# Kernel optimization log

Measured on AMD Instinct MI355X. Metric: run time of the kernel, lower is better.

The kernel has to match this reference:

```python
import jax, jax.numpy as jnp
import numpy as np

N = 50000      # nodes
E = 800000     # edges
F_IN = 128     # numInputFeatures
HID = 64       # numHiddenLayerFeatures
C = 40         # numClasses


def setup_inputs() -> dict:
    key = jax.random.key(0)
    ks = jax.random.split(key, 24)
    def nrm(k, shape, s=0.05):
        return jax.random.normal(k, shape, jnp.float32) * s
    return {
        "x": jax.random.normal(ks[0], (N, F_IN), jnp.float32),
        "edge_index": jax.random.randint(ks[1], (2, E), 0, N, jnp.int64),
        "w": jax.random.normal(ks[2], (3,), jnp.float32),  # ensemble weights
        # GCNConv
        "W_gcn": nrm(ks[3], (F_IN, HID)), "b_gcn": jnp.zeros((HID,), jnp.float32),
        # SAGEConv (lin_l on aggregated neighbors w/ bias, lin_r on root no bias)
        "Wl_sage": nrm(ks[4], (F_IN, HID)), "bl_sage": jnp.zeros((HID,), jnp.float32),
        "Wr_sage": nrm(ks[5], (F_IN, HID)),
        # GATConv heads=1
        "W_gat": nrm(ks[6], (F_IN, HID)), "att_src": nrm(ks[7], (HID,)),
        "att_dst": nrm(ks[8], (HID,)), "b_gat": jnp.zeros((HID,), jnp.float32),
        # TransformerConv heads=1 (hidden -> classes)
        "Wq": nrm(ks[9], (HID, C)), "bq": jnp.zeros((C,), jnp.float32),
        "Wk": nrm(ks[10], (HID, C)), "bk": jnp.zeros((C,), jnp.float32),
        "Wv": nrm(ks[11], (HID, C)), "bv": jnp.zeros((C,), jnp.float32),
        "Wskip": nrm(ks[12], (HID, C)), "bskip": jnp.zeros((C,), jnp.float32),
    }


def _segment_softmax(e, seg, num_segments):
    m = jax.ops.segment_max(e, seg, num_segments=num_segments)
    ex = jnp.exp(e - m[seg])
    s = jax.ops.segment_sum(ex, seg, num_segments=num_segments)
    return ex / (s[seg] + 1e-16)


def _gcn(x, src, dst, W, b):
    h = x @ W                                        # [N, HID]
    loop = jnp.arange(N, dtype=src.dtype)
    s = jnp.concatenate([src, loop]); d = jnp.concatenate([dst, loop])
    deg = jax.ops.segment_sum(jnp.ones_like(d, jnp.float32), d, num_segments=N)
    dinv = jnp.where(deg > 0, jax.lax.rsqrt(deg), 0.0)
    norm = dinv[s] * dinv[d]                         # [E+N]
    out = jax.ops.segment_sum(h[s] * norm[:, None], d, num_segments=N)
    return out + b


def _sage(x, src, dst, Wl, bl, Wr):
    cnt = jax.ops.segment_sum(jnp.ones((src.shape[0],), jnp.float32), dst, num_segments=N)
    agg = jax.ops.segment_sum(x[src], dst, num_segments=N) / jnp.maximum(cnt, 1.0)[:, None]
    return agg @ Wl + bl + x @ Wr


def _gat(x, src, dst, W, att_src, att_dst, b):
    h = x @ W                                        # [N, HID]
    loop = jnp.arange(N, dtype=src.dtype)
    s = jnp.concatenate([src, loop]); d = jnp.concatenate([dst, loop])
    a_s = h @ att_src; a_d = h @ att_dst             # [N]
    e = jax.nn.leaky_relu(a_s[s] + a_d[d], 0.2)
    alpha = _segment_softmax(e, d, N)
    out = jax.ops.segment_sum(alpha[:, None] * h[s], d, num_segments=N)
    return out + b


def _transformer(x, src, dst, Wq, bq, Wk, bk, Wv, bv, Wskip, bskip):
    q = x @ Wq + bq; k = x @ Wk + bk; v = x @ Wv + bv  # [N, C]
    score = jnp.sum(q[dst] * k[src], axis=-1) / jnp.sqrt(jnp.float32(C))
    alpha = _segment_softmax(score, dst, N)
    out = jax.ops.segment_sum(alpha[:, None] * v[src], dst, num_segments=N)
    return out + (x @ Wskip + bskip)


def reference(x, edge_index, w, W_gcn, b_gcn, Wl_sage, bl_sage, Wr_sage,
              W_gat, att_src, att_dst, b_gat,
              Wq, bq, Wk, bk, Wv, bv, Wskip, bskip):
    src, dst = edge_index[0], edge_index[1]
    gelu = lambda t: jax.nn.gelu(t, approximate=False)
    ens = gelu(_gcn(x, src, dst, W_gcn, b_gcn)) * w[0]
    ens = ens + gelu(_sage(x, src, dst, Wl_sage, bl_sage, Wr_sage)) * w[1]
    ens = ens + gelu(_gat(x, src, dst, W_gat, att_src, att_dst, b_gat)) * w[2]
    out = _transformer(ens, src, dst, Wq, bq, Wk, bk, Wv, bv, Wskip, bskip)
    return jax.nn.log_softmax(out, axis=1)
```

## Files before the change

kernel.cpp:

```cpp
#include <hip/hip_runtime.h>
#include <math.h>

#define NN 50000
#define EE 800000
#define FIN 128
#define HID 64
#define CL 40
#define SCB 256
#define NBLK ((NN + SCB - 1) / SCB)
#define NREP 8

typedef unsigned short ushort_t;
typedef unsigned int uint_t;
typedef float f32x4 __attribute__((ext_vector_type(4)));
typedef short s16x8 __attribute__((ext_vector_type(8)));

__device__ __forceinline__ ushort_t f2bf(float f) {
  uint_t u = __float_as_uint(f);
  u = (u + 0x7FFFu + ((u >> 16) & 1u)) >> 16;
  return (ushort_t)u;
}
__device__ __forceinline__ uint_t f2bf2(float lo, float hi) {
  return (uint_t)f2bf(lo) | ((uint_t)f2bf(hi) << 16);
}
__device__ __forceinline__ float bf2f(ushort_t s) {
  return __uint_as_float(((uint_t)s) << 16);
}
__device__ __forceinline__ float bflo(uint_t u) {
  return __uint_as_float(u << 16);
}
__device__ __forceinline__ float bfhi(uint_t u) {
  return __uint_as_float(u & 0xFFFF0000u);
}

__device__ __forceinline__ int wave_sum_i(int v) {
#pragma unroll
  for (int off = 32; off > 0; off >>= 1) v += __shfl_xor(v, off, 64);
  return v;
}
__device__ __forceinline__ float half_sum(float v) {
#pragma unroll
  for (int off = 16; off > 0; off >>= 1) v += __shfl_xor(v, off, 64);
  return v;
}
__device__ __forceinline__ float half_max(float v) {
#pragma unroll
  for (int off = 16; off > 0; off >>= 1) v = fmaxf(v, __shfl_xor(v, off, 64));
  return v;
}
__device__ __forceinline__ float gelu_exact(float x) {
  return 0.5f * x * (1.0f + erff(x * 0.70710678118654752f));
}
__device__ __forceinline__ float leaky02(float x) {
  return x >= 0.f ? x : 0.2f * x;
}

#define PREP_CAST 6250
#define PREP_W 169
#define PREP_HIST 3125
__global__ __launch_bounds__(256) void k_prep(
    const float* __restrict__ x, const int* __restrict__ dst,
    const float* __restrict__ W0, const float* __restrict__ W1,
    const float* __restrict__ W2, const float* __restrict__ W3,
    const float* __restrict__ Q0, const float* __restrict__ Q1,
    const float* __restrict__ Q2, const float* __restrict__ Q3,
    const float* __restrict__ b0, const float* __restrict__ b1,
    const float* __restrict__ b2, const float* __restrict__ b3,
    ushort_t* __restrict__ xb, ushort_t* __restrict__ WtA,
    ushort_t* __restrict__ WtB, float* __restrict__ bcat,
    int* __restrict__ cntR, int* __restrict__ erank) {
  int b = blockIdx.x, t = threadIdx.x;
  if (b < PREP_CAST) {
    int i = b * 256 + t;
    if (i < NN * FIN / 4) {
      float4 v = ((const float4*)x)[i];
      ushort4 o;
      o.x = f2bf(v.x); o.y = f2bf(v.y); o.z = f2bf(v.z); o.w = f2bf(v.w);
      ((ushort4*)xb)[i] = o;
    }
  } else if (b < PREP_CAST + PREP_W) {
    int idx = (b - PREP_CAST) * 256 + t;
    if (idx < 32768) {
      int m = idx >> 13, r = idx & 8191, c = r >> 7, k = r & 127;
      const float* W = (m == 0) ? W0 : (m == 1) ? W1 : (m == 2) ? W2 : W3;
      WtA[idx] = f2bf(W[k * HID + c]);
    } else if (idx < 43008) {
      int j = idx - 32768;
      int c = j >> 6, k = j & 63;
      int mm = c / CL, cc = c % CL;
      const float* W = (mm == 0) ? Q0 : (mm == 1) ? Q1 : (mm == 2) ? Q2 : Q3;
      WtB[j] = f2bf(W[k * CL + cc]);
    } else if (idx < 43168) {
      int c = idx - 43008;
      int mm = c / CL, cc = c % CL;
      const float* bb = (mm == 0) ? b0 : (mm == 1) ? b1 : (mm == 2) ? b2 : b3;
      bcat[c] = bb[cc];
    }
  } else {
    int hb = b - PREP_CAST - PREP_W;
    int e = hb * 256 + t;
    if (e < EE) {
      int r = hb & (NREP - 1);
      erank[e] = atomicAdd(&cntR[(size_t)r * NN + dst[e]], 1);
    }
  }
}

__global__ __launch_bounds__(256) void k_gemmA(
    const ushort_t* __restrict__ xb, const ushort_t* __restrict__ WtA,
    const float* __restrict__ attS, const float* __restrict__ attD,
    ushort_t* __restrict__ Hb, float* __restrict__ a_s,
    float* __restrict__ a_d) {
  __shared__ __align__(16) ushort_t wlds[64 * 136];
  const int t = threadIdx.x;
  const int m = blockIdx.y;
  for (int idx = t; idx < 64 * 16; idx += 256) {
    int c = idx >> 4, ch = idx & 15;
    *(uint4*)&wlds[c * 136 + ch * 8] =
        *(const uint4*)(WtA + m * 8192 + c * 128 + ch * 8);
  }
  __syncthreads();
  const int wv = t >> 6, l = t & 63;
  const int lr = l & 15, lg = l >> 4;
  const int rbase = blockIdx.x * 64 + wv * 16;
  int arow = rbase + lr;
  int arowc = arow < NN ? arow : NN - 1;
  const ushort_t* ap = xb + (size_t)arowc * 128 + lg * 8;
  f32x4 acc[4] = {};
#pragma unroll
  for (int ks = 0; ks < 4; ++ks) {
    s16x8 af = *(const s16x8*)(ap + ks * 32);
#pragma unroll
    for (int n = 0; n < 4; ++n) {
      s16x8 bf = *(const s16x8*)&wlds[(n * 16 + lr) * 136 + ks * 32 + lg * 8];
      acc[n] = __builtin_amdgcn_mfma_f32_16x16x32_bf16(af, bf, acc[n], 0, 0, 0);
    }
  }
#pragma unroll
  for (int n = 0; n < 4; ++n) {
#pragma unroll
    for (int j = 0; j < 4; ++j) {
      int orow = rbase + lg * 4 + j;
      if (orow < NN)
        Hb[(size_t)orow * 256 + m * 64 + n * 16 + lr] = f2bf(acc[n][j]);
    }
  }
  if (m == 2) {
    float sat[4], dat[4];
#pragma unroll
    for (int n = 0; n < 4; ++n) {
      sat[n] = attS[n * 16 + lr];
      dat[n] = attD[n * 16 + lr];
    }
#pragma unroll
    for (int j = 0; j < 4; ++j) {
      float ps = 0.f, pd = 0.f;
#pragma unroll
      for (int n = 0; n < 4; ++n) {
        ps = fmaf(acc[n][j], sat[n], ps);
        pd = fmaf(acc[n][j], dat[n], pd);
      }
#pragma unroll
      for (int off = 1; off < 16; off <<= 1) {
        ps += __shfl_xor(ps, off, 64);
        pd += __shfl_xor(pd, off, 64);
      }
      int orow = rbase + lg * 4 + j;
      if (lr == 0 && orow < NN) { a_s[orow] = ps; a_d[orow] = pd; }
    }
  }
}

__global__ __launch_bounds__(SCB) void k_bsum(const int* __restrict__ cntR,
                                              int* __restrict__ bsum) {
  __shared__ int wsm[4];
  int i = blockIdx.x * SCB + threadIdx.x;
  int v = 0;
  if (i < NN) {
#pragma unroll
    for (int r = 0; r < NREP; ++r) v += cntR[(size_t)r * NN + i];
  }
  int s = wave_sum_i(v);
  int lane = threadIdx.x & 63, wv = threadIdx.x >> 6;
  if (lane == 0) wsm[wv] = s;
  __syncthreads();
  if (threadIdx.x == 0) bsum[blockIdx.x] = wsm[0] + wsm[1] + wsm[2] + wsm[3];
}

__global__ __launch_bounds__(SCB) void k_scanapply(
    const int* __restrict__ cntR, const int* __restrict__ bsum,
    int* __restrict__ cnt, int* __restrict__ offs, int* __restrict__ base8,
    float* __restrict__ dinv) {
  __shared__ int ts[SCB];
  __shared__ int wred[4];
  int b = blockIdx.x, t = threadIdx.x;
  int pv = (t < b) ? bsum[t] : 0;
  int ps = wave_sum_i(pv);
  int lane = t & 63, wv = t >> 6;
  if (lane == 0) wred[wv] = ps;
  int i = b * SCB + t;
  int cr[NREP];
  int v = 0;
  if (i < NN) {
#pragma unroll
    for (int r = 0; r < NREP; ++r) {
      cr[r] = cntR[(size_t)r * NN + i];
      v += cr[r];
    }
  }
  ts[t] = v;
  __syncthreads();
  int prefix = wred[0] + wred[1] + wred[2] + wred[3];
  for (int off = 1; off < SCB; off <<= 1) {
    int u = (t >= off) ? ts[t - off] : 0;
    __syncthreads();
    ts[t] += u;
    __syncthreads();
  }
  if (i < NN) {
    int ex = ts[t] - v + prefix;
    offs[i] = ex;
    cnt[i] = v;
    dinv[i] = rsqrtf((float)v + 1.0f);
    int run = ex;
#pragma unroll
    for (int r = 0; r < NREP; ++r) {
      base8[(size_t)i * NREP + r] = run;
      run += cr[r];
    }
  }
}

__global__ __launch_bounds__(256) void k_sc1(const int* __restrict__ dst,
                                             const int* __restrict__ erank,
                                             const int* __restrict__ base8,
                                             int* __restrict__ esorted) {
  int e = blockIdx.x * blockDim.x + threadIdx.x;
  if (e < EE) {
    int d = dst[e];
    int r = (e >> 8) & (NREP - 1);
    esorted[base8[(size_t)d * NREP + r] + erank[e]] = e;
  }
}

__global__ __launch_bounds__(256) void k_sc2(
    const int* __restrict__ esorted, const int* __restrict__ src,
    const int* __restrict__ dst, const float* __restrict__ a_s,
    const float* __restrict__ a_d, const float* __restrict__ dinv,
    int* __restrict__ srcidx, int* __restrict__ dsts,
    float2* __restrict__ edata) {
  int p = blockIdx.x * blockDim.x + threadIdx.x;
  if (p < EE) {
    int e = esorted[p];
    int s = src[e], d = dst[e];
    srcidx[p] = s;
    dsts[p] = d;
    float ex = __expf(leaky02(a_s[s] + a_d[d]));
    edata[p] = make_float2(dinv[s] * dinv[d], ex);
  }
}

__global__ __launch_bounds__(256) void k_agg1(
    const int* __restrict__ srcidx, const int* __restrict__ offs,
    const int* __restrict__ cnt, const ushort_t* __restrict__ Hb,
    const float2* __restrict__ edata, const float* __restrict__ dinv,
    const float* __restrict__ a_s, const float* __restrict__ a_d,
    const float* __restrict__ b_gcn, const float* __restrict__ bl,
    const float* __restrict__ b_gat, const float* __restrict__ w,
    ushort_t* __restrict__ ensb) {
  int node = (blockIdx.x * blockDim.x + threadIdx.x) >> 6;
  int lane = threadIdx.x & 63;
  if (node >= NN) return;
  const int half = lane >> 5;
  const int fl = lane & 31;
  int beg = offs[node];
  int c = cnt[node];
  int end = beg + c;
  float ag0 = 0.f, ag1 = 0.f, as0 = 0.f, as1 = 0.f, aa0 = 0.f, aa1 = 0.f,
        dg = 0.f;
  int p = beg + half;
  for (; p + 6 < end; p += 8) {
    int sA = srcidx[p], sB = srcidx[p + 2], sC = srcidx[p + 4],
        sD = srcidx[p + 6];
    float2 eA = edata[p], eB = edata[p + 2], eC = edata[p + 4],
           eD = edata[p + 6];
    const uint_t* hA = (const uint_t*)(Hb + (size_t)sA * 256);
    const uint_t* hB = (const uint_t*)(Hb + (size_t)sB * 256);
    const uint_t* hC = (const uint_t*)(Hb + (size_t)sC * 256);
    const uint_t* hD = (const uint_t*)(Hb + (size_t)sD * 256);
    uint_t gA = hA[fl], qA = hA[32 + fl], tA = hA[64 + fl];
    uint_t gB = hB[fl], qB = hB[32 + fl], tB = hB[64 + fl];
    uint_t gC = hC[fl], qC = hC[32 + fl], tC = hC[64 + fl];
    uint_t gD = hD[fl], qD = hD[32 + fl], tD = hD[64 + fl];
    ag0 = fmaf(bflo(gA), eA.x, ag0); ag1 = fmaf(bfhi(gA), eA.x, ag1);
    ag0 = fmaf(bflo(gB), eB.x, ag0); ag1 = fmaf(bfhi(gB), eB.x, ag1);
    ag0 = fmaf(bflo(gC), eC.x, ag0); ag1 = fmaf(bfhi(gC), eC.x, ag1);
    ag0 = fmaf(bflo(gD), eD.x, ag0); ag1 = fmaf(bfhi(gD), eD.x, ag1);
    as0 += (bflo(qA) + bflo(qB)) + (bflo(qC) + bflo(qD));
    as1 += (bfhi(qA) + bfhi(qB)) + (bfhi(qC) + bfhi(qD));
    aa0 = fmaf(bflo(tA), eA.y, aa0); aa1 = fmaf(bfhi(tA), eA.y, aa1);
    aa0 = fmaf(bflo(tB), eB.y, aa0); aa1 = fmaf(bfhi(tB), eB.y, aa1);
    aa0 = fmaf(bflo(tC), eC.y, aa0); aa1 = fmaf(bfhi(tC), eC.y, aa1);
    aa0 = fmaf(bflo(tD), eD.y, aa0); aa1 = fmaf(bfhi(tD), eD.y, aa1);
    dg += (eA.y + eB.y) + (eC.y + eD.y);
  }
  for (; p < end; p += 2) {
    int sA = srcidx[p];
    float2 eA = edata[p];
    const uint_t* hA = (const uint_t*)(Hb + (size_t)sA * 256);
    uint_t gA = hA[fl], qA = hA[32 + fl], tA = hA[64 + fl];
    ag0 = fmaf(bflo(gA), eA.x, ag0); ag1 = fmaf(bfhi(gA), eA.x, ag1);
    as0 += bflo(qA);                 as1 += bfhi(qA);
    aa0 = fmaf(bflo(tA), eA.y, aa0); aa1 = fmaf(bfhi(tA), eA.y, aa1);
    dg += eA.y;
  }
  ag0 += __shfl_xor(ag0, 32, 64); ag1 += __shfl_xor(ag1, 32, 64);
  as0 += __shfl_xor(as0, 32, 64); as1 += __shfl_xor(as1, 32, 64);
  aa0 += __shfl_xor(aa0, 32, 64); aa1 += __shfl_xor(aa1, 32, 64);
  dg += __shfl_xor(dg, 32, 64);
  float dd = dinv[node];
  float exl = __expf(leaky02(a_s[node] + a_d[node]));
  const uint_t* hd = (const uint_t*)(Hb + (size_t)node * 256);
  uint_t hg = hd[fl], ht = hd[64 + fl], hr = hd[96 + fl];
  float2 bg = ((const float2*)b_gcn)[fl];
  float2 bs = ((const float2*)bl)[fl];
  float2 ba = ((const float2*)b_gat)[fl];
  float dd2 = dd * dd;
  float cinv = 1.0f / fmaxf((float)c, 1.0f);
  float gdi = 1.0f / (dg + exl + 1e-16f);
  float g0 = ag0 + dd2 * bflo(hg) + bg.x;
  float g1 = ag1 + dd2 * bfhi(hg) + bg.y;
  float s0 = as0 * cinv + bs.x + bflo(hr);
  float s1 = as1 * cinv + bs.y + bfhi(hr);
  float t0 = (aa0 + exl * bflo(ht)) * gdi + ba.x;
  float t1 = (aa1 + exl * bfhi(ht)) * gdi + ba.y;
  float w0 = w[0], w1 = w[1], w2 = w[2];
  float e0 = w0 * gelu_exact(g0) + w1 * gelu_exact(s0) + w2 * gelu_exact(t0);
  float e1 = w0 * gelu_exact(g1) + w1 * gelu_exact(s1) + w2 * gelu_exact(t1);
  if (half == 0) ((uint_t*)ensb)[(size_t)node * 32 + fl] = f2bf2(e0, e1);
}

__global__ __launch_bounds__(256) void k_gemmB(
    const ushort_t* __restrict__ ensb, const ushort_t* __restrict__ WtB,
    const float* __restrict__ bcat, ushort_t* __restrict__ QKVSb) {
  __shared__ __align__(16) ushort_t wb[160 * 72];
  __shared__ float bsh[160];
  const int t = threadIdx.x;
  for (int idx = t; idx < 160 * 8; idx += 256) {
    int c = idx >> 3, ch = idx & 7;
    *(uint4*)&wb[c * 72 + ch * 8] = *(const uint4*)(WtB + c * 64 + ch * 8);
  }
  if (t < 160) bsh[t] = bcat[t];
  __syncthreads();
  const int wv = t >> 6, l = t & 63;
  const int lr = l & 15, lg = l >> 4;
  const int rbase = blockIdx.x * 64 + wv * 16;
  int arow = rbase + lr;
  int arowc = arow < NN ? arow : NN - 1;
  const ushort_t* ap = ensb + (size_t)arowc * 64 + lg * 8;
  f32x4 acc[10] = {};
#pragma unroll
  for (int ks = 0; ks < 2; ++ks) {
    s16x8 af = *(const s16x8*)(ap + ks * 32);
#pragma unroll
    for (int n = 0; n < 10; ++n) {
      s16x8 bf = *(const s16x8*)&wb[(n * 16 + lr) * 72 + ks * 32 + lg * 8];
      acc[n] = __builtin_amdgcn_mfma_f32_16x16x32_bf16(af, bf, acc[n], 0, 0, 0);
    }
  }
#pragma unroll
  for (int n = 0; n < 10; ++n) {
    int col = n * 16 + lr;
#pragma unroll
    for (int j = 0; j < 4; ++j) {
      int orow = rbase + lg * 4 + j;
      if (orow < NN)
        QKVSb[(size_t)orow * 160 + col] = f2bf(acc[n][j] + bsh[col]);
    }
  }
}

__global__ __launch_bounds__(256) void k_score(
    const int* __restrict__ srcidx, const int* __restrict__ dsts,
    const ushort_t* __restrict__ QKVSb, float* __restrict__ escore) {
  int p = (blockIdx.x * 256 + threadIdx.x) >> 3;
  int l = threadIdx.x & 7;
  if (p >= EE) return;
  int s = srcidx[p], d = dsts[p];
  float part = 0.f;
  if (l < 5) {
    const uint4 qv = *(const uint4*)(QKVSb + (size_t)d * 160 + l * 8);
    const uint4 kv = *(const uint4*)(QKVSb + (size_t)s * 160 + 40 + l * 8);
    part = bflo(qv.x) * bflo(kv.x);
    part = fmaf(bfhi(qv.x), bfhi(kv.x), part);
    part = fmaf(bflo(qv.y), bflo(kv.y), part);
    part = fmaf(bfhi(qv.y), bfhi(kv.y), part);
    part = fmaf(bflo(qv.z), bflo(kv.z), part);
    part = fmaf(bfhi(qv.z), bfhi(kv.z), part);
    part = fmaf(bflo(qv.w), bflo(kv.w), part);
    part = fmaf(bfhi(qv.w), bfhi(kv.w), part);
  }
  part += __shfl_xor(part, 1, 64);
  part += __shfl_xor(part, 2, 64);
  part += __shfl_xor(part, 4, 64);
  if (l == 0) escore[p] = __expf(part * 0.15811388300841897f);
}

__global__ __launch_bounds__(256) void k_agg2(
    const int* __restrict__ srcidx, const int* __restrict__ offs,
    const int* __restrict__ cnt, const ushort_t* __restrict__ QKVSb,
    const float* __restrict__ escore, float* __restrict__ out) {
  int node = (blockIdx.x * blockDim.x + threadIdx.x) >> 6;
  int lane = threadIdx.x & 63;
  if (node >= NN) return;
  const int half = lane >> 5;
  const int fl = lane & 31;
  const bool valid = fl < 20;
  int beg = offs[node];
  int end = beg + cnt[node];
  float den = 0.f, av0 = 0.f, av1 = 0.f;
  int p = beg + half;
  for (; p + 6 < end; p += 8) {
    int sA = srcidx[p], sB = srcidx[p + 2], sC = srcidx[p + 4],
        sD = srcidx[p + 6];
    float eA = escore[p], eB = escore[p + 2], eC = escore[p + 4],
          eD = escore[p + 6];
    uint_t vA = valid ? ((const uint_t*)(QKVSb + (size_t)sA * 160))[40 + fl] : 0u;
    uint_t vB = valid ? ((const uint_t*)(QKVSb + (size_t)sB * 160))[40 + fl] : 0u;
    uint_t vC = valid ? ((const uint_t*)(QKVSb + (size_t)sC * 160))[40 + fl] : 0u;
    uint_t vD = valid ? ((const uint_t*)(QKVSb + (size_t)sD * 160))[40 + fl] : 0u;
    av0 = fmaf(eA, bflo(vA), av0); av1 = fmaf(eA, bfhi(vA), av1);
    av0 = fmaf(eB, bflo(vB), av0); av1 = fmaf(eB, bfhi(vB), av1);
    av0 = fmaf(eC, bflo(vC), av0); av1 = fmaf(eC, bfhi(vC), av1);
    av0 = fmaf(eD, bflo(vD), av0); av1 = fmaf(eD, bfhi(vD), av1);
    den += (eA + eB) + (eC + eD);
  }
  for (; p < end; p += 2) {
    int sA = srcidx[p];
    float eA = escore[p];
    uint_t vA = valid ? ((const uint_t*)(QKVSb + (size_t)sA * 160))[40 + fl] : 0u;
    av0 = fmaf(eA, bflo(vA), av0); av1 = fmaf(eA, bfhi(vA), av1);
    den += eA;
  }
  av0 += __shfl_xor(av0, 32, 64);
  av1 += __shfl_xor(av1, 32, 64);
  den += __shfl_xor(den, 32, 64);
  const uint_t* rd = (const uint_t*)(QKVSb + (size_t)node * 160);
  uint_t sk = valid ? rd[60 + fl] : 0u;
  float di = 1.0f / (den + 1e-16f);
  float o0 = valid ? av0 * di + bflo(sk) : -3.0e38f;
  float o1 = valid ? av1 * di + bfhi(sk) : -3.0e38f;
  float m = half_max(fmaxf(o0, o1));
  float eo = valid ? __expf(o0 - m) + __expf(o1 - m) : 0.f;
  float ls = logf(half_sum(eo));
  if (valid && half == 0) {
    float2 r = make_float2(o0 - m - ls, o1 - m - ls);
    ((float2*)out)[(size_t)node * 20 + fl] = r;
  }
}

extern "C" void kernel_launch(void* const* d_in, const int* in_sizes, int n_in,
                              void* d_out, int out_size, void* d_ws,
                              size_t ws_size, hipStream_t stream) {
  const float* x     = (const float*)d_in[0];
  const int*   ei    = (const int*)d_in[1];
  const float* w     = (const float*)d_in[2];
  const float* W_gcn = (const float*)d_in[3];
  const float* b_gcn = (const float*)d_in[4];
  const float* Wl    = (const float*)d_in[5];
  const float* bl    = (const float*)d_in[6];
  const float* Wr    = (const float*)d_in[7];
  const float* W_gat = (const float*)d_in[8];
  const float* att_s = (const float*)d_in[9];
  const float* att_d = (const float*)d_in[10];
  const float* b_gat = (const float*)d_in[11];
  const float* Wq    = (const float*)d_in[12];
  const float* bq    = (const float*)d_in[13];
  const float* Wk    = (const float*)d_in[14];
  const float* bk    = (const float*)d_in[15];
  const float* Wv    = (const float*)d_in[16];
  const float* bv    = (const float*)d_in[17];
  const float* Wsk   = (const float*)d_in[18];
  const float* bsk   = (const float*)d_in[19];
  float* out = (float*)d_out;
  float* ws  = (float*)d_ws;

  const int* src = ei;
  const int* dst = ei + EE;

  ushort_t* Hb     = (ushort_t*)ws;
  ushort_t* ensb   = (ushort_t*)(ws + (size_t)128 * NN);
  float*    a_s    = ws + (size_t)160 * NN;
  float*    a_d    = ws + (size_t)161 * NN;
  float*    dinv   = ws + (size_t)162 * NN;
  ushort_t* qkvsb  = (ushort_t*)(ws + (size_t)163 * NN);
  ushort_t* xb     = (ushort_t*)(ws + (size_t)243 * NN);
  ushort_t* WtA    = (ushort_t*)(ws + (size_t)307 * NN);
  ushort_t* WtB    = (ushort_t*)(ws + (size_t)307 * NN + 16384);
  float*    bcat   = ws + (size_t)307 * NN + 21504;
  float*    escore = ws + (size_t)307 * NN + 21664;
  float2*   edata  = (float2*)(ws + (size_t)307 * NN + 21664 + EE);
  int*      ibase  = (int*)(ws + (size_t)307 * NN + 21664 + 3 * (size_t)EE);
  int*      cnt    = ibase;
  int*      offs   = ibase + NN;
  int*      srcidx = ibase + 2 * NN;
  int*      dsts   = ibase + 2 * NN + EE;
  int*      erank  = ibase + 2 * NN + 2 * EE;
  int*      esorted= ibase + 2 * NN + 3 * EE;
  int*      bsum   = ibase + 2 * NN + 4 * EE;
  int*      cntR   = ibase + 2 * NN + 4 * EE + 256;
  int*      base8  = cntR + (size_t)NREP * NN;

  hipMemsetAsync(cntR, 0, (size_t)NREP * NN * sizeof(int), stream);

  k_prep<<<PREP_CAST + PREP_W + PREP_HIST, 256, 0, stream>>>(
      x, dst, W_gcn, Wl, W_gat, Wr, Wq, Wk, Wv, Wsk, bq, bk, bv, bsk, xb, WtA,
      WtB, bcat, cntR, erank);

  dim3 gA((NN + 63) / 64, 4);
  k_gemmA<<<gA, 256, 0, stream>>>(xb, WtA, att_s, att_d, Hb, a_s, a_d);
  k_bsum<<<NBLK, SCB, 0, stream>>>(cntR, bsum);
  k_scanapply<<<NBLK, SCB, 0, stream>>>(cntR, bsum, cnt, offs, base8, dinv);
  k_sc1<<<(EE + 255) / 256, 256, 0, stream>>>(dst, erank, base8, esorted);
  k_sc2<<<(EE + 255) / 256, 256, 0, stream>>>(esorted, src, dst, a_s, a_d,
                                              dinv, srcidx, dsts, edata);
  k_agg1<<<(NN + 3) / 4, 256, 0, stream>>>(srcidx, offs, cnt, Hb, edata, dinv,
                                           a_s, a_d, b_gcn, bl, b_gat, w, ensb);
  k_gemmB<<<(NN + 63) / 64, 256, 0, stream>>>(ensb, WtB, bcat, qkvsb);
  k_score<<<(EE * 8 + 255) / 256, 256, 0, stream>>>(srcidx, dsts, qkvsb,
                                                    escore);
  k_agg2<<<(NN + 3) / 4, 256, 0, stream>>>(srcidx, offs, cnt, qkvsb, escore,
                                           out);
}
```

Measured before the change: 217.1 us.

## Fuse gemmA column blocks, pack edge aux data, pad QKVS rows to aligned segments

k_gemmA now runs one block per 64-row tile that loads the A fragments once and loops over all four weight slices in two LDS-staged halves. Before, four blockIdx.y blocks each reloaded the same x rows. k_scanapply writes packed float2 (dinv, a_s/a_d) arrays, so k_sc2 does two gathers per edge instead of four. The Q/K/V/skip buffer is padded from 160 to 256 bf16 per row, with each segment aligned to 64 elements for aligned vector loads in the score and aggregation kernels. This costs more workspace and write traffic for the padded rows, and fewer gemmA blocks in flight.

```diff
diff --git a/kernel.cpp b/kernel.cpp
--- a/kernel.cpp
+++ b/kernel.cpp
@@ -9,6 +9,7 @@
 #define SCB 256
 #define NBLK ((NN + SCB - 1) / SCB)
 #define NREP 8
+#define QW 256
 
 typedef unsigned short ushort_t;
 typedef unsigned int uint_t;
@@ -111,62 +112,71 @@
     const float* __restrict__ attS, const float* __restrict__ attD,
     ushort_t* __restrict__ Hb, float* __restrict__ a_s,
     float* __restrict__ a_d) {
-  __shared__ __align__(16) ushort_t wlds[64 * 136];
+  __shared__ __align__(16) ushort_t wlds[2 * 64 * 136];
   const int t = threadIdx.x;
-  const int m = blockIdx.y;
-  for (int idx = t; idx < 64 * 16; idx += 256) {
-    int c = idx >> 4, ch = idx & 15;
-    *(uint4*)&wlds[c * 136 + ch * 8] =
-        *(const uint4*)(WtA + m * 8192 + c * 128 + ch * 8);
-  }
-  __syncthreads();
   const int wv = t >> 6, l = t & 63;
   const int lr = l & 15, lg = l >> 4;
   const int rbase = blockIdx.x * 64 + wv * 16;
   int arow = rbase + lr;
   int arowc = arow < NN ? arow : NN - 1;
   const ushort_t* ap = xb + (size_t)arowc * 128 + lg * 8;
-  f32x4 acc[4] = {};
-#pragma unroll
-  for (int ks = 0; ks < 4; ++ks) {
-    s16x8 af = *(const s16x8*)(ap + ks * 32);
-#pragma unroll
-    for (int n = 0; n < 4; ++n) {
-      s16x8 bf = *(const s16x8*)&wlds[(n * 16 + lr) * 136 + ks * 32 + lg * 8];
-      acc[n] = __builtin_amdgcn_mfma_f32_16x16x32_bf16(af, bf, acc[n], 0, 0, 0);
-    }
-  }
-#pragma unroll
-  for (int n = 0; n < 4; ++n) {
-#pragma unroll
-    for (int j = 0; j < 4; ++j) {
-      int orow = rbase + lg * 4 + j;
-      if (orow < NN)
-        Hb[(size_t)orow * 256 + m * 64 + n * 16 + lr] = f2bf(acc[n][j]);
-    }
-  }
-  if (m == 2) {
-    float sat[4], dat[4];
-#pragma unroll
-    for (int n = 0; n < 4; ++n) {
-      sat[n] = attS[n * 16 + lr];
-      dat[n] = attD[n * 16 + lr];
-    }
-#pragma unroll
-    for (int j = 0; j < 4; ++j) {
-      float ps = 0.f, pd = 0.f;
+  s16x8 af[4];
+#pragma unroll
+  for (int ks = 0; ks < 4; ++ks) af[ks] = *(const s16x8*)(ap + ks * 32);
+  for (int hf = 0; hf < 2; ++hf) {
+    if (hf) __syncthreads();
+    for (int idx = t; idx < 2 * 64 * 16; idx += 256) {
+      int mm = idx >> 10, r2 = idx & 1023, c = r2 >> 4, ch = r2 & 15;
+      *(uint4*)&wlds[(mm * 64 + c) * 136 + ch * 8] =
+          *(const uint4*)(WtA + (hf * 2 + mm) * 8192 + c * 128 + ch * 8);
+    }
+    __syncthreads();
+    for (int mm = 0; mm < 2; ++mm) {
+      int m = hf * 2 + mm;
+      f32x4 acc[4] = {};
+#pragma unroll
+      for (int ks = 0; ks < 4; ++ks) {
+#pragma unroll
+        for (int n = 0; n < 4; ++n) {
+          s16x8 bf = *(const s16x8*)&wlds[(mm * 64 + n * 16 + lr) * 136 +
+                                          ks * 32 + lg * 8];
+          acc[n] =
+              __builtin_amdgcn_mfma_f32_16x16x32_bf16(af[ks], bf, acc[n], 0, 0, 0);
+        }
+      }
 #pragma unroll
       for (int n = 0; n < 4; ++n) {
-        ps = fmaf(acc[n][j], sat[n], ps);
-        pd = fmaf(acc[n][j], dat[n], pd);
+#pragma unroll
+        for (int j = 0; j < 4; ++j) {
+          int orow = rbase + lg * 4 + j;
+          if (orow < NN)
+            Hb[(size_t)orow * 256 + m * 64 + n * 16 + lr] = f2bf(acc[n][j]);
+        }
       }
-#pragma unroll
-      for (int off = 1; off < 16; off <<= 1) {
-        ps += __shfl_xor(ps, off, 64);
-        pd += __shfl_xor(pd, off, 64);
+      if (m == 2) {
+        float sat[4], dat[4];
+#pragma unroll
+        for (int n = 0; n < 4; ++n) {
+          sat[n] = attS[n * 16 + lr];
+          dat[n] = attD[n * 16 + lr];
+        }
+#pragma unroll
+        for (int j = 0; j < 4; ++j) {
+          float ps = 0.f, pd = 0.f;
+#pragma unroll
+          for (int n = 0; n < 4; ++n) {
+            ps = fmaf(acc[n][j], sat[n], ps);
+            pd = fmaf(acc[n][j], dat[n], pd);
+          }
+#pragma unroll
+          for (int off = 1; off < 16; off <<= 1) {
+            ps += __shfl_xor(ps, off, 64);
+            pd += __shfl_xor(pd, off, 64);
+          }
+          int orow = rbase + lg * 4 + j;
+          if (lr == 0 && orow < NN) { a_s[orow] = ps; a_d[orow] = pd; }
+        }
       }
-      int orow = rbase + lg * 4 + j;
-      if (lr == 0 && orow < NN) { a_s[orow] = ps; a_d[orow] = pd; }
     }
   }
 }
@@ -189,8 +199,10 @@
 
 __global__ __launch_bounds__(SCB) void k_scanapply(
     const int* __restrict__ cntR, const int* __restrict__ bsum,
+    const float* __restrict__ a_s, const float* __restrict__ a_d,
     int* __restrict__ cnt, int* __restrict__ offs, int* __restrict__ base8,
-    float* __restrict__ dinv) {
+    float* __restrict__ dinv, float2* __restrict__ auxS,
+    float2* __restrict__ auxD) {
   __shared__ int ts[SCB];
   __shared__ int wred[4];
   int b = blockIdx.x, t = threadIdx.x;
@@ -221,7 +233,10 @@
     int ex = ts[t] - v + prefix;
     offs[i] = ex;
     cnt[i] = v;
-    dinv[i] = rsqrtf((float)v + 1.0f);
+    float dv = rsqrtf((float)v + 1.0f);
+    dinv[i] = dv;
+    auxS[i] = make_float2(dv, a_s[i]);
+    auxD[i] = make_float2(dv, a_d[i]);
     int run = ex;
 #pragma unroll
     for (int r = 0; r < NREP; ++r) {
@@ -245,18 +260,19 @@
 
 __global__ __launch_bounds__(256) void k_sc2(
     const int* __restrict__ esorted, const int* __restrict__ src,
-    const int* __restrict__ dst, const float* __restrict__ a_s,
-    const float* __restrict__ a_d, const float* __restrict__ dinv,
-    int* __restrict__ srcidx, int* __restrict__ dsts,
-    float2* __restrict__ edata) {
+    const int* __restrict__ dst, const float2* __restrict__ auxS,
+    const float2* __restrict__ auxD, int* __restrict__ srcidx,
+    int* __restrict__ dsts, float2* __restrict__ edata) {
   int p = blockIdx.x * blockDim.x + threadIdx.x;
   if (p < EE) {
     int e = esorted[p];
     int s = src[e], d = dst[e];
     srcidx[p] = s;
     dsts[p] = d;
-    float ex = __expf(leaky02(a_s[s] + a_d[d]));
-    edata[p] = make_float2(dinv[s] * dinv[d], ex);
+    float2 A = auxS[s];
+    float2 B = auxD[d];
+    float ex = __expf(leaky02(A.y + B.y));
+    edata[p] = make_float2(A.x * B.x, ex);
   }
 }
 
@@ -371,11 +387,13 @@
 #pragma unroll
   for (int n = 0; n < 10; ++n) {
     int col = n * 16 + lr;
+    int seg = col / CL;
+    int off = seg * 64 + (col - seg * CL);
 #pragma unroll
     for (int j = 0; j < 4; ++j) {
       int orow = rbase + lg * 4 + j;
       if (orow < NN)
-        QKVSb[(size_t)orow * 160 + col] = f2bf(acc[n][j] + bsh[col]);
+        QKVSb[(size_t)orow * QW + off] = f2bf(acc[n][j] + bsh[col]);
     }
   }
 }
@@ -389,8 +407,8 @@
   int s = srcidx[p], d = dsts[p];
   float part = 0.f;
   if (l < 5) {
-    const uint4 qv = *(const uint4*)(QKVSb + (size_t)d * 160 + l * 8);
-    const uint4 kv = *(const uint4*)(QKVSb + (size_t)s * 160 + 40 + l * 8);
+    const uint4 qv = *(const uint4*)(QKVSb + (size_t)d * QW + l * 8);
+    const uint4 kv = *(const uint4*)(QKVSb + (size_t)s * QW + 64 + l * 8);
     part = bflo(qv.x) * bflo(kv.x);
     part = fmaf(bfhi(qv.x), bfhi(kv.x), part);
     part = fmaf(bflo(qv.y), bflo(kv.y), part);
@@ -419,16 +437,17 @@
   int beg = offs[node];
   int end = beg + cnt[node];
   float den = 0.f, av0 = 0.f, av1 = 0.f;
+  const int VOFF = 64;
   int p = beg + half;
   for (; p + 6 < end; p += 8) {
     int sA = srcidx[p], sB = srcidx[p + 2], sC = srcidx[p + 4],
         sD = srcidx[p + 6];
     float eA = escore[p], eB = escore[p + 2], eC = escore[p + 4],
           eD = escore[p + 6];
-    uint_t vA = valid ? ((const uint_t*)(QKVSb + (size_t)sA * 160))[40 + fl] : 0u;
-    uint_t vB = valid ? ((const uint_t*)(QKVSb + (size_t)sB * 160))[40 + fl] : 0u;
-    uint_t vC = valid ? ((const uint_t*)(QKVSb + (size_t)sC * 160))[40 + fl] : 0u;
-    uint_t vD = valid ? ((const uint_t*)(QKVSb + (size_t)sD * 160))[40 + fl] : 0u;
+    uint_t vA = valid ? ((const uint_t*)QKVSb)[(size_t)sA * 128 + VOFF + fl] : 0u;
+    uint_t vB = valid ? ((const uint_t*)QKVSb)[(size_t)sB * 128 + VOFF + fl] : 0u;
+    uint_t vC = valid ? ((const uint_t*)QKVSb)[(size_t)sC * 128 + VOFF + fl] : 0u;
+    uint_t vD = valid ? ((const uint_t*)QKVSb)[(size_t)sD * 128 + VOFF + fl] : 0u;
     av0 = fmaf(eA, bflo(vA), av0); av1 = fmaf(eA, bfhi(vA), av1);
     av0 = fmaf(eB, bflo(vB), av0); av1 = fmaf(eB, bfhi(vB), av1);
     av0 = fmaf(eC, bflo(vC), av0); av1 = fmaf(eC, bfhi(vC), av1);
@@ -438,15 +457,14 @@
   for (; p < end; p += 2) {
     int sA = srcidx[p];
     float eA = escore[p];
-    uint_t vA = valid ? ((const uint_t*)(QKVSb + (size_t)sA * 160))[40 + fl] : 0u;
+    uint_t vA = valid ? ((const uint_t*)QKVSb)[(size_t)sA * 128 + VOFF + fl] : 0u;
     av0 = fmaf(eA, bflo(vA), av0); av1 = fmaf(eA, bfhi(vA), av1);
     den += eA;
   }
   av0 += __shfl_xor(av0, 32, 64);
   av1 += __shfl_xor(av1, 32, 64);
   den += __shfl_xor(den, 32, 64);
-  const uint_t* rd = (const uint_t*)(QKVSb + (size_t)node * 160);
-  uint_t sk = valid ? rd[60 + fl] : 0u;
+  uint_t sk = valid ? ((const uint_t*)QKVSb)[(size_t)node * 128 + 96 + fl] : 0u;
   float di = 1.0f / (den + 1e-16f);
   float o0 = valid ? av0 * di + bflo(sk) : -3.0e38f;
   float o1 = valid ? av1 * di + bfhi(sk) : -3.0e38f;
@@ -494,13 +512,15 @@
   float*    a_d    = ws + (size_t)161 * NN;
   float*    dinv   = ws + (size_t)162 * NN;
   ushort_t* qkvsb  = (ushort_t*)(ws + (size_t)163 * NN);
-  ushort_t* xb     = (ushort_t*)(ws + (size_t)243 * NN);
-  ushort_t* WtA    = (ushort_t*)(ws + (size_t)307 * NN);
-  ushort_t* WtB    = (ushort_t*)(ws + (size_t)307 * NN + 16384);
-  float*    bcat   = ws + (size_t)307 * NN + 21504;
-  float*    escore = ws + (size_t)307 * NN + 21664;
-  float2*   edata  = (float2*)(ws + (size_t)307 * NN + 21664 + EE);
-  int*      ibase  = (int*)(ws + (size_t)307 * NN + 21664 + 3 * (size_t)EE);
+  ushort_t* xb     = (ushort_t*)(ws + (size_t)291 * NN);
+  ushort_t* WtA    = (ushort_t*)(ws + (size_t)355 * NN);
+  ushort_t* WtB    = (ushort_t*)(ws + (size_t)355 * NN + 16384);
+  float*    bcat   = ws + (size_t)355 * NN + 21504;
+  float*    escore = ws + (size_t)355 * NN + 21664;
+  float2*   edata  = (float2*)(ws + (size_t)355 * NN + 21664 + EE);
+  float2*   auxS   = (float2*)(ws + (size_t)355 * NN + 21664 + 3 * (size_t)EE);
+  float2*   auxD   = auxS + NN;
+  int*      ibase  = (int*)(ws + (size_t)359 * NN + 21664 + 3 * (size_t)EE);
   int*      cnt    = ibase;
   int*      offs   = ibase + NN;
   int*      srcidx = ibase + 2 * NN;
@@ -517,13 +537,14 @@
       x, dst, W_gcn, Wl, W_gat, Wr, Wq, Wk, Wv, Wsk, bq, bk, bv, bsk, xb, WtA,
       WtB, bcat, cntR, erank);
 
-  dim3 gA((NN + 63) / 64, 4);
-  k_gemmA<<<gA, 256, 0, stream>>>(xb, WtA, att_s, att_d, Hb, a_s, a_d);
+  k_gemmA<<<(NN + 63) / 64, 256, 0, stream>>>(xb, WtA, att_s, att_d, Hb, a_s,
+                                              a_d);
   k_bsum<<<NBLK, SCB, 0, stream>>>(cntR, bsum);
-  k_scanapply<<<NBLK, SCB, 0, stream>>>(cntR, bsum, cnt, offs, base8, dinv);
+  k_scanapply<<<NBLK, SCB, 0, stream>>>(cntR, bsum, a_s, a_d, cnt, offs, base8,
+                                        dinv, auxS, auxD);
   k_sc1<<<(EE + 255) / 256, 256, 0, stream>>>(dst, erank, base8, esorted);
-  k_sc2<<<(EE + 255) / 256, 256, 0, stream>>>(esorted, src, dst, a_s, a_d,
-                                              dinv, srcidx, dsts, edata);
+  k_sc2<<<(EE + 255) / 256, 256, 0, stream>>>(esorted, src, dst, auxS, auxD,
+                                              srcidx, dsts, edata);
   k_agg1<<<(NN + 3) / 4, 256, 0, stream>>>(srcidx, offs, cnt, Hb, edata, dinv,
                                            a_s, a_d, b_gcn, bl, b_gat, w, ensb);
   k_gemmB<<<(NN + 63) / 64, 256, 0, stream>>>(ensb, WtB, bcat, qkvsb);
```

After: 224.5 us. +3.4%, slower.
